# Performance work log

Hardware: AMD Instinct MI355X
Metric: run time of the kernel (lower is better)

Reference implementation:

```python
import jax, jax.numpy as jnp
import numpy as np
import math

R = 16            # input_resolution (window side)
N = R * R         # tokens per window
H = 16            # num_heads
D = 32            # head_dim
SCALE = D ** -0.5

def _rel_pos_index(r):
    # Swin-style relative position index, [N, N] int
    coords = np.stack(np.meshgrid(np.arange(r), np.arange(r), indexing='ij'))  # [2,r,r]
    cf = coords.reshape(2, -1)                          # [2, N]
    rel = cf[:, :, None] - cf[:, None, :]               # [2, N, N]
    rel = rel.transpose(1, 2, 0).astype(np.int64)       # [N, N, 2]
    rel[:, :, 0] += r - 1
    rel[:, :, 1] += r - 1
    rel[:, :, 0] *= 2 * r - 1
    return rel.sum(-1)                                  # [N, N]

def _modulation(n, k):
    # cosine-distance modulation matrix, [n*n, n*n]
    idx = np.arange(n * n)
    rr, cc = idx // n, idx % n
    d = np.sqrt((rr[:, None] - rr[None, :]) ** 2 + (cc[:, None] - cc[None, :]) ** 2)
    T = 4 * (n - 1) * math.sqrt(2)
    f = 2 * math.pi / T
    m = np.exp(np.cos(f * d)) / 2
    if k % n == 0:
        k = k - 1
    bound = m[0, k]
    m = np.where(m < bound, 0.0, m)
    return jnp.asarray(m, jnp.float32)

_REL_IDX = jnp.asarray(_rel_pos_index(R))   # [N, N] int
_MOD = _modulation(R, 3 * R)                 # [N, N] float (eval-mode local modulation)

def setup_inputs() -> dict:
    key = jax.random.key(0)
    ks = jax.random.split(key, 6)
    C = H * D
    return {
        'x': jax.random.normal(ks[0], (128, N, C), jnp.float32),
        'qkv_w': jax.random.normal(ks[1], (3 * C, C), jnp.float32) * 0.02,
        'qkv_b': jax.random.normal(ks[2], (3 * C,), jnp.float32) * 0.02,
        'proj_w': jax.random.normal(ks[3], (C, C), jnp.float32) * 0.02,
        'proj_b': jax.random.normal(ks[4], (C,), jnp.float32) * 0.02,
        'rpb_table': jax.random.normal(ks[5], ((2 * R - 1) ** 2, H), jnp.float32) * 0.02,
    }

def reference(x, qkv_w, qkv_b, proj_w, proj_b, rpb_table):
    B, n, C = x.shape
    # qkv projection: torch Linear is x @ W^T + b
    qkv = x @ qkv_w.T + qkv_b                       # [B, N, 3C]
    qkv = qkv.reshape(B, n, 3, H, D)
    q = qkv[:, :, 0].transpose(0, 2, 1, 3) * SCALE  # [B, H, N, D]
    k = qkv[:, :, 1].transpose(0, 2, 1, 3)
    v = qkv[:, :, 2].transpose(0, 2, 1, 3)
    attn = jnp.einsum('bhnd,bhmd->bhnm', q, k)      # [B, H, N, N]
    bias = rpb_table[_REL_IDX]                      # [N, N, H]
    attn = attn + bias.transpose(2, 0, 1)[None]     # + [1, H, N, N]
    attn = jax.nn.softmax(attn, axis=-1)
    attn = attn * _MOD[None, None]                  # local eval-mode modulation
    out = jnp.einsum('bhnm,bhmd->bhnd', attn, v)    # [B, H, N, D]
    out = out.transpose(0, 2, 1, 3).reshape(B, n, C)
    return out @ proj_w.T + proj_b
```

## Files before the change

kernel.cpp:

```cpp
#include <hip/hip_runtime.h>
#include <hip/hip_bf16.h>

typedef unsigned short u16;
typedef unsigned int u32;
typedef __bf16 bf16x8 __attribute__((ext_vector_type(8)));
typedef float f32x4 __attribute__((ext_vector_type(4)));

#define AS1(p) ((const __attribute__((address_space(1))) void*)(p))
#define AS3(p) ((__attribute__((address_space(3))) void*)(p))

#define TOK   256
#define CDIM  512
#define QKVC  1536
#define LOG2E 1.4426950408889634f
#define QSCALE (0.17677669529663687f * 1.4426950408889634f)

__device__ __forceinline__ u16 f2b(float f) {
  unsigned u = __float_as_uint(f);
  unsigned r = (u + 0x7fffu + ((u >> 16) & 1u)) >> 16;
  return (u16)r;
}
__device__ __forceinline__ u16 f2bc(float f) {
  __bf16 h = (__bf16)f;
  u16 u;
  __builtin_memcpy(&u, &h, 2);
  return u;
}
__device__ __forceinline__ float bf_lo(u32 wd) { return __uint_as_float(wd << 16); }
__device__ __forceinline__ float bf_hi(u32 wd) { return __uint_as_float(wd & 0xffff0000u); }
__device__ __forceinline__ float ex2(float x) {
  float r;
  asm("v_exp_f32 %0, %1" : "=v"(r) : "v"(x));
  return r;
}

__global__ __launch_bounds__(256) void cvt_bf16_kernel(const float* __restrict__ in,
                                                       u16* __restrict__ out, int n) {
  int i = (blockIdx.x * 256 + threadIdx.x) * 8;
  if (i >= n) return;
  float4 a = *(const float4*)(in + i);
  float4 b = *(const float4*)(in + i + 4);
  u16 h[8];
  h[0] = f2b(a.x); h[1] = f2b(a.y); h[2] = f2b(a.z); h[3] = f2b(a.w);
  h[4] = f2b(b.x); h[5] = f2b(b.y); h[6] = f2b(b.z); h[7] = f2b(b.w);
  *(uint4*)(out + i) = *(const uint4*)h;
}

__global__ __launch_bounds__(256) void build_bias2_kernel(const float* __restrict__ rpb,
                                                          u16* __restrict__ bias2) {
  int i = blockIdx.x * 256 + threadIdx.x;
  int tr = i & 63, lane = (i >> 6) & 63, rb = (i >> 12) & 15, h = i >> 16;
  int t = tr >> 2, r = tr & 3;
  int n = rb * 16 + (lane & 15);
  int m = t * 16 + (lane >> 4) * 4 + r;
  int idx = ((n >> 4) - (m >> 4) + 15) * 31 + ((n & 15) - (m & 15) + 15);
  bias2[i] = f2b(rpb[idx * 16 + h] * LOG2E);
}

__global__ __launch_bounds__(256) void build_mod2_kernel(u16* __restrict__ mod2) {
  int i = blockIdx.x * 256 + threadIdx.x;
  int tr = i & 63, lane = (i >> 6) & 63, rb = i >> 12;
  int t = tr >> 2, r = tr & 3;
  int n = rb * 16 + (lane & 15);
  int m = t * 16 + (lane >> 4) * 4 + r;
  int dr = (n >> 4) - (m >> 4), dc = (n & 15) - (m & 15);
  int d2 = dr * dr + dc * dc;
  float val = 0.0f;
  if (d2 <= 229) {
    const float fc = 6.2831853071795864f / (60.0f * 1.4142135623730951f);
    val = expf(cosf(fc * sqrtf((float)d2))) * 0.5f;
  }
  mod2[i] = f2b(val);
}

template<int MODE>
__global__ __launch_bounds__(MODE == 0 ? 512 : 256) void gemm_bt(
    const float* __restrict__ Ax, const u16* __restrict__ A,
    const u16* __restrict__ Bt, const float* __restrict__ bvec,
    u16* __restrict__ oq, u16* __restrict__ ok, u16* __restrict__ ov,
    float* __restrict__ of) {
  constexpr int K = 512;
  constexpr int BM = (MODE == 0) ? 256 : 128;
  constexpr int NT = (MODE == 0) ? 512 : 256;
  constexpr int NBN = (MODE == 0) ? 12 : 4;
  constexpr int PER_XCD = (MODE == 0) ? 192 : 128;
  __shared__ __align__(16) u16 SM[(MODE == 0) ? 32768 : 16384];
  u16* As = SM;
  u16* Bs = SM + BM * 64;
  const int tid = threadIdx.x, lane = tid & 63, w = tid >> 6;
  const int wr = w >> 1, wc = w & 1, lr = lane & 15, lg = lane >> 4;
  const int logical = (blockIdx.x & 7) * PER_XCD + (blockIdx.x >> 3);
  const int bm = (logical / (2 * NBN)) * 2 + (logical & 1);
  const int bn = (logical % (2 * NBN)) >> 1;
  const u16* Bg = Bt + (size_t)bn * 128 * K;
  f32x4 acc[4][4];
#pragma unroll
  for (int m = 0; m < 4; ++m)
#pragma unroll
    for (int n = 0; n < 4; ++n) acc[m][n] = (f32x4){0.f, 0.f, 0.f, 0.f};

  for (int k0 = 0; k0 < K; k0 += 64) {
    if (MODE == 0) {
#pragma unroll
      for (int it = 0; it < 4; ++it) {
        int chunk = it * NT + tid;
        int r = chunk >> 3, kc = chunk & 7;
        int gg = kc ^ (r & 7);
        const float* src = Ax + (size_t)(bm * 256 + r) * K + k0 + gg * 8;
        float4 v0 = *(const float4*)src;
        float4 v1 = *(const float4*)(src + 4);
        u16 hb[8];
        hb[0] = f2bc(v0.x); hb[1] = f2bc(v0.y); hb[2] = f2bc(v0.z); hb[3] = f2bc(v0.w);
        hb[4] = f2bc(v1.x); hb[5] = f2bc(v1.y); hb[6] = f2bc(v1.z); hb[7] = f2bc(v1.w);
        *(uint4*)(As + chunk * 8) = *(const uint4*)hb;
      }
#pragma unroll
      for (int it = 0; it < 2; ++it) {
        int chunk = it * NT + tid;
        int r = chunk >> 3, kc = chunk & 7;
        int kcs = kc ^ (r & 7);
        __builtin_amdgcn_global_load_lds(AS1(Bg + (size_t)r * K + k0 + kcs * 8),
                                         AS3(Bs + chunk * 8), 16, 0, 0);
      }
    } else {
      const u16* Ag = A + (size_t)bm * 128 * K;
#pragma unroll
      for (int it = 0; it < 4; ++it) {
        int chunk = it * NT + tid;
        int r = chunk >> 3, kc = chunk & 7;
        int kcs = kc ^ (r & 7);
        __builtin_amdgcn_global_load_lds(AS1(Ag + (size_t)r * K + k0 + kcs * 8),
                                         AS3(As + chunk * 8), 16, 0, 0);
        __builtin_amdgcn_global_load_lds(AS1(Bg + (size_t)r * K + k0 + kcs * 8),
                                         AS3(Bs + chunk * 8), 16, 0, 0);
      }
    }
    __syncthreads();
#pragma unroll
    for (int kk = 0; kk < 2; ++kk) {
      bf16x8 a[4], b[4];
#pragma unroll
      for (int m = 0; m < 4; ++m) {
        int ar = wr * 64 + m * 16 + lr;
        a[m] = *(const bf16x8*)&As[ar * 64 + (((kk * 4 + lg) ^ (lr & 7)) << 3)];
      }
#pragma unroll
      for (int n = 0; n < 4; ++n) {
        int br = wc * 64 + n * 16 + lr;
        b[n] = *(const bf16x8*)&Bs[br * 64 + (((kk * 4 + lg) ^ (lr & 7)) << 3)];
      }
#pragma unroll
      for (int m = 0; m < 4; ++m)
#pragma unroll
        for (int n = 0; n < 4; ++n)
          acc[m][n] = __builtin_amdgcn_mfma_f32_16x16x32_bf16(a[m], b[n], acc[m][n], 0, 0, 0);
    }
    __syncthreads();
  }

  if (MODE == 1) {
#pragma unroll
    for (int m = 0; m < 4; ++m)
#pragma unroll
      for (int n = 0; n < 4; ++n)
#pragma unroll
        for (int r = 0; r < 4; ++r) {
          int row = bm * BM + wr * 64 + m * 16 + lg * 4 + r;
          int col = bn * 128 + wc * 64 + n * 16 + lr;
          of[(size_t)row * CDIM + col] = acc[m][n][r] + bvec[col];
        }
    return;
  }

  const int typ = bn >> 2;
  const int col0 = bn * 128 + wc * 64;
  const int row0 = bm * 256 + wr * 64;
  char* Tb = (char*)SM + w * 8192;

#pragma unroll
  for (int n = 0; n < 4; ++n) {
    float bv = bvec[col0 + n * 16 + lr];
#pragma unroll
    for (int m = 0; m < 4; ++m)
#pragma unroll
      for (int r = 0; r < 4; ++r) {
        float v = acc[m][n][r] + bv;
        if (typ == 0) v *= QSCALE;
        int row_l, col_l;
        if (typ < 2) { row_l = m * 16 + lg * 4 + r; col_l = n * 16 + lr; }
        else         { row_l = n * 16 + lr;         col_l = m * 16 + lg * 4 + r; }
        int byte = row_l * 128 + ((((col_l >> 3) ^ (row_l & 7)) << 4) | ((col_l & 7) << 1));
        *(u16*)(Tb + byte) = f2b(v);
      }
  }
  asm volatile("" ::: "memory");
  if (typ < 2) {
    int tok = row0 + lane;
    int tokb = tok >> 8;
    u16* obase = (typ == 0) ? oq : ok;
#pragma unroll
    for (int G = 0; G < 8; ++G) {
      int hl = G >> 2, q = G & 3;
      uint4 v = *(const uint4*)(Tb + lane * 128 + ((G ^ (lane & 7)) << 4));
      int hh = ((col0 >> 5) & 15) + hl;
      size_t a = ((((size_t)tokb * 16 + hh) * 16 + ((tok >> 4) & 15)) * 64 +
                  ((tok & 15) | (q << 4))) * 8;
      *(uint4*)(obase + a) = v;
    }
  } else {
    int tl0 = row0 & 255, tokb = row0 >> 8;
    int hl = lane >> 5, t = (lane >> 3) & 3, c = lane & 7;
    int hh = ((col0 >> 5) & 15) + hl;
#pragma unroll
    for (int i = 0; i < 8; ++i) {
      int d = i * 4 + t;
      uint4 v = *(const uint4*)(Tb + (hl * 32 + d) * 128 + (c << 4));
      size_t a = (((size_t)tokb * 16 + hh) * 32 + d) * 256 + tl0 + c * 8;
      *(uint4*)(ov + a) = v;
    }
  }
}

__global__ __launch_bounds__(512, 4) void attn_kernel(const u16* __restrict__ qfrag,
                                                      const u16* __restrict__ kfrag,
                                                      const u16* __restrict__ vsw,
                                                      const u16* __restrict__ bias2,
                                                      const u16* __restrict__ mod2,
                                                      u16* __restrict__ attnout) {
  __shared__ __align__(16) u16 SM[24576];
  const int logical = (blockIdx.x & 7) * 512 + (blockIdx.x >> 3);
  const int h = logical >> 8;
  const int b = (logical >> 1) & 127;
  const int qpair = logical & 1;
  const int tid = threadIdx.x, lane = tid & 63, w = tid >> 6;
  const int lr = lane & 15, lg = lane >> 4;
  const int rb = qpair * 8 + w;
  const int bhid = b * 16 + h;

  const u16* kg = kfrag + (size_t)bhid * 8192;
  const u16* vg = vsw + (size_t)bhid * 8192;
#pragma unroll
  for (int it = 0; it < 2; ++it) {
    __builtin_amdgcn_global_load_lds(AS1(kg + (it * 512 + tid) * 8),
                                     AS3(SM + (it * 512 + tid) * 8), 16, 0, 0);
    __builtin_amdgcn_global_load_lds(AS1(vg + (it * 512 + tid) * 8),
                                     AS3(SM + 8192 + (it * 512 + tid) * 8), 16, 0, 0);
  }
  bf16x8 qf = *(const bf16x8*)(qfrag + ((size_t)bhid * 16 + rb) * 512 + lane * 8);
  __syncthreads();

  const u16* bias_base = bias2 + (((size_t)h * 16 + rb) * 64 + lane) * 64;
  const u16* mod_base  = mod2 + ((size_t)rb * 64 + lane) * 64;
  char* Pbase = (char*)SM + 32768 + w * 2048;
  const char* Vb = (const char*)(SM + 8192);

  f32x4 s[16];
#pragma unroll
  for (int q = 0; q < 4; ++q) {
    u32 bw8[8];
    {
      const uint4* bp = (const uint4*)(bias_base + q * 16);
      *(uint4*)&bw8[0] = bp[0]; *(uint4*)&bw8[4] = bp[1];
    }
#pragma unroll
    for (int tl = 0; tl < 4; ++tl) {
      int t = q * 4 + tl;
      bf16x8 kf = *(const bf16x8*)(SM + (t * 64 + lane) * 8);
      f32x4 c;
      c[0] = bf_lo(bw8[tl * 2]);     c[1] = bf_hi(bw8[tl * 2]);
      c[2] = bf_lo(bw8[tl * 2 + 1]); c[3] = bf_hi(bw8[tl * 2 + 1]);
      s[t] = __builtin_amdgcn_mfma_f32_16x16x32_bf16(kf, qf, c, 0, 0, 0);
    }
  }

  float mr0 = s[0][0], mr1 = s[0][1], mr2 = s[0][2], mr3 = s[0][3];
#pragma unroll
  for (int t = 1; t < 16; ++t) {
    mr0 = fmaxf(mr0, s[t][0]); mr1 = fmaxf(mr1, s[t][1]);
    mr2 = fmaxf(mr2, s[t][2]); mr3 = fmaxf(mr3, s[t][3]);
  }
  float mx = fmaxf(fmaxf(mr0, mr1), fmaxf(mr2, mr3));
  mx = fmaxf(mx, __shfl_xor(mx, 16, 64));
  mx = fmaxf(mx, __shfl_xor(mx, 32, 64));
  float s0 = 0.f, s1 = 0.f, s2 = 0.f, s3 = 0.f;
#pragma unroll
  for (int t = 0; t < 16; ++t) {
    s[t][0] = ex2(s[t][0] - mx); s0 += s[t][0];
    s[t][1] = ex2(s[t][1] - mx); s1 += s[t][1];
    s[t][2] = ex2(s[t][2] - mx); s2 += s[t][2];
    s[t][3] = ex2(s[t][3] - mx); s3 += s[t][3];
  }
  float sm = (s0 + s1) + (s2 + s3);
  sm += __shfl_xor(sm, 16, 64);
  sm += __shfl_xor(sm, 32, 64);
  sm = __builtin_amdgcn_rcpf(sm);

  f32x4 o0 = (f32x4){0.f, 0.f, 0.f, 0.f};
  f32x4 o1 = (f32x4){0.f, 0.f, 0.f, 0.f};
#pragma unroll
  for (int q = 0; q < 4; ++q) {
    u32 mw8[8];
    {
      const uint4* mp = (const uint4*)(mod_base + q * 16);
      *(uint4*)&mw8[0] = mp[0]; *(uint4*)&mw8[4] = mp[1];
    }
#pragma unroll
    for (int tl = 0; tl < 4; ++tl) {
      int t = q * 4 + tl;
      u16 pk[4];
#pragma unroll
      for (int r = 0; r < 4; ++r) {
        u32 wd = mw8[tl * 2 + (r >> 1)];
        float mf = (r & 1) ? bf_hi(wd) : bf_lo(wd);
        pk[r] = f2bc(s[t][r] * sm * mf);
      }
      int hi2 = (t * 2 + (lg >> 1)) & 3;
      *(uint2*)(Pbase + ((t >> 1) & 1) * 1024 + ((hi2 << 4) | lr) * 16 + (lg & 1) * 8)
          = *(const uint2*)pk;
    }
    asm volatile("" ::: "memory");
#pragma unroll
    for (int kl = 0; kl < 2; ++kl) {
      bf16x8 pa = *(const bf16x8*)(Pbase + kl * 1024 + lane * 16);
      int cv = ((q * 2 + kl) * 4 + lg) ^ (lr & 7);
      bf16x8 v0 = *(const bf16x8*)(Vb + lr * 512 + cv * 16);
      bf16x8 v1 = *(const bf16x8*)(Vb + (16 + lr) * 512 + cv * 16);
      o0 = __builtin_amdgcn_mfma_f32_16x16x32_bf16(pa, v0, o0, 0, 0, 0);
      o1 = __builtin_amdgcn_mfma_f32_16x16x32_bf16(pa, v1, o1, 0, 0, 0);
    }
    asm volatile("" ::: "memory");
  }

  u16* orow = attnout + (size_t)(b * TOK + rb * 16) * CDIM + h * 32;
#pragma unroll
  for (int r = 0; r < 4; ++r) {
    orow[(size_t)(lg * 4 + r) * CDIM + lr] = f2bc(o0[r]);
    orow[(size_t)(lg * 4 + r) * CDIM + 16 + lr] = f2bc(o1[r]);
  }
}

extern "C" void kernel_launch(void* const* d_in, const int* in_sizes, int n_in,
                              void* d_out, int out_size, void* d_ws, size_t ws_size,
                              hipStream_t stream) {
  const float* x      = (const float*)d_in[0];
  const float* qkv_w  = (const float*)d_in[1];
  const float* qkv_b  = (const float*)d_in[2];
  const float* proj_w = (const float*)d_in[3];
  const float* proj_b = (const float*)d_in[4];
  const float* rpb    = (const float*)d_in[5];

  char* ws = (char*)d_ws;
  u16* qkvwb  = (u16*)(ws + 33554432);
  u16* projwb = (u16*)(ws + 35127296);
  u16* qfrag  = (u16*)(ws + 35651584);
  u16* kfrag  = (u16*)(ws + 69206016);
  u16* vswb   = (u16*)(ws + 102760448);
  u16* attnb  = (u16*)(ws + 136314880);
  u16* bias2  = (u16*)(ws + 169869312);
  u16* mod2   = (u16*)(ws + 171966464);

  cvt_bf16_kernel<<<384, 256, 0, stream>>>(qkv_w, qkvwb, 1536 * 512);
  cvt_bf16_kernel<<<128, 256, 0, stream>>>(proj_w, projwb, 512 * 512);
  build_bias2_kernel<<<4096, 256, 0, stream>>>(rpb, bias2);
  build_mod2_kernel<<<256, 256, 0, stream>>>(mod2);

  gemm_bt<0><<<1536, 512, 0, stream>>>(x, nullptr, qkvwb, qkv_b,
                                       qfrag, kfrag, vswb, nullptr);
  attn_kernel<<<4096, 512, 0, stream>>>(qfrag, kfrag, vswb, bias2, mod2, attnb);
  gemm_bt<1><<<1024, 256, 0, stream>>>(nullptr, attnb, projwb, proj_b,
                                       nullptr, nullptr, nullptr, (float*)d_out);
}
```

Baseline: 214.6 us.

## Software-pipeline QKV GEMM with register prefetch of x and double-buffered weight tiles

In the QKV projection GEMM (MODE 0), the next k-step's fp32 activation tile is prefetched into registers and the next weight tile is loaded asynchronously into a second LDS buffer while MFMAs run on the current step. This is meant to hide global load latency behind compute instead of stalling at each k-step. It raises register pressure from holding 8 float4 per thread and uses LDS space that was previously unused. The output-projection GEMM path is unchanged apart from renaming.

```diff
diff --git a/kernel.cpp b/kernel.cpp
--- a/kernel.cpp
+++ b/kernel.cpp
@@ -86,7 +86,8 @@
   constexpr int PER_XCD = (MODE == 0) ? 192 : 128;
   __shared__ __align__(16) u16 SM[(MODE == 0) ? 32768 : 16384];
   u16* As = SM;
-  u16* Bs = SM + BM * 64;
+  u16* Bs0 = SM + BM * 64;
+  u16* Bs1 = (MODE == 0) ? (SM + BM * 64 + 8192) : Bs0;
   const int tid = threadIdx.x, lane = tid & 63, w = tid >> 6;
   const int wr = w >> 1, wc = w & 1, lr = lane & 15, lg = lane >> 4;
   const int logical = (blockIdx.x & 7) * PER_XCD + (blockIdx.x >> 3);
@@ -99,63 +100,111 @@
 #pragma unroll
     for (int n = 0; n < 4; ++n) acc[m][n] = (f32x4){0.f, 0.f, 0.f, 0.f};
 
-  for (int k0 = 0; k0 < K; k0 += 64) {
-    if (MODE == 0) {
+  if (MODE == 0) {
+    float4 ar0[4], ar1[4];
+#pragma unroll
+    for (int it = 0; it < 4; ++it) {
+      int chunk = it * NT + tid;
+      int r = chunk >> 3, gg = (chunk & 7) ^ (r & 7);
+      const float* src = Ax + (size_t)(bm * 256 + r) * K + gg * 8;
+      ar0[it] = *(const float4*)src;
+      ar1[it] = *(const float4*)(src + 4);
+    }
+#pragma unroll
+    for (int it = 0; it < 2; ++it) {
+      int chunk = it * NT + tid;
+      int r = chunk >> 3, kcs = (chunk & 7) ^ (r & 7);
+      __builtin_amdgcn_global_load_lds(AS1(Bg + (size_t)r * K + kcs * 8),
+                                       AS3(Bs0 + chunk * 8), 16, 0, 0);
+    }
+#pragma unroll 1
+    for (int ks = 0; ks < 8; ++ks) {
+      const int k0 = ks * 64;
+      u16* Bcur = (ks & 1) ? Bs1 : Bs0;
+      u16* Bnxt = (ks & 1) ? Bs0 : Bs1;
 #pragma unroll
       for (int it = 0; it < 4; ++it) {
         int chunk = it * NT + tid;
-        int r = chunk >> 3, kc = chunk & 7;
-        int gg = kc ^ (r & 7);
-        const float* src = Ax + (size_t)(bm * 256 + r) * K + k0 + gg * 8;
-        float4 v0 = *(const float4*)src;
-        float4 v1 = *(const float4*)(src + 4);
         u16 hb[8];
-        hb[0] = f2bc(v0.x); hb[1] = f2bc(v0.y); hb[2] = f2bc(v0.z); hb[3] = f2bc(v0.w);
-        hb[4] = f2bc(v1.x); hb[5] = f2bc(v1.y); hb[6] = f2bc(v1.z); hb[7] = f2bc(v1.w);
+        hb[0] = f2bc(ar0[it].x); hb[1] = f2bc(ar0[it].y);
+        hb[2] = f2bc(ar0[it].z); hb[3] = f2bc(ar0[it].w);
+        hb[4] = f2bc(ar1[it].x); hb[5] = f2bc(ar1[it].y);
+        hb[6] = f2bc(ar1[it].z); hb[7] = f2bc(ar1[it].w);
         *(uint4*)(As + chunk * 8) = *(const uint4*)hb;
       }
-#pragma unroll
-      for (int it = 0; it < 2; ++it) {
-        int chunk = it * NT + tid;
-        int r = chunk >> 3, kc = chunk & 7;
-        int kcs = kc ^ (r & 7);
-        __builtin_amdgcn_global_load_lds(AS1(Bg + (size_t)r * K + k0 + kcs * 8),
-                                         AS3(Bs + chunk * 8), 16, 0, 0);
-      }
-    } else {
-      const u16* Ag = A + (size_t)bm * 128 * K;
+      __syncthreads();
+      if (ks < 7) {
+#pragma unroll
+        for (int it = 0; it < 2; ++it) {
+          int chunk = it * NT + tid;
+          int r = chunk >> 3, kcs = (chunk & 7) ^ (r & 7);
+          __builtin_amdgcn_global_load_lds(AS1(Bg + (size_t)r * K + k0 + 64 + kcs * 8),
+                                           AS3(Bnxt + chunk * 8), 16, 0, 0);
+        }
+#pragma unroll
+        for (int it = 0; it < 4; ++it) {
+          int chunk = it * NT + tid;
+          int r = chunk >> 3, gg = (chunk & 7) ^ (r & 7);
+          const float* src = Ax + (size_t)(bm * 256 + r) * K + k0 + 64 + gg * 8;
+          ar0[it] = *(const float4*)src;
+          ar1[it] = *(const float4*)(src + 4);
+        }
+      }
+#pragma unroll
+      for (int kk = 0; kk < 2; ++kk) {
+        bf16x8 a[4], b[4];
+#pragma unroll
+        for (int m = 0; m < 4; ++m) {
+          int ar = wr * 64 + m * 16 + lr;
+          a[m] = *(const bf16x8*)&As[ar * 64 + (((kk * 4 + lg) ^ (lr & 7)) << 3)];
+        }
+#pragma unroll
+        for (int n = 0; n < 4; ++n) {
+          int br = wc * 64 + n * 16 + lr;
+          b[n] = *(const bf16x8*)&Bcur[br * 64 + (((kk * 4 + lg) ^ (lr & 7)) << 3)];
+        }
+#pragma unroll
+        for (int m = 0; m < 4; ++m)
+#pragma unroll
+          for (int n = 0; n < 4; ++n)
+            acc[m][n] = __builtin_amdgcn_mfma_f32_16x16x32_bf16(a[m], b[n], acc[m][n], 0, 0, 0);
+      }
+      __syncthreads();
+    }
+  } else {
+    const u16* Ag = A + (size_t)bm * 128 * K;
+    for (int k0 = 0; k0 < K; k0 += 64) {
 #pragma unroll
       for (int it = 0; it < 4; ++it) {
         int chunk = it * NT + tid;
-        int r = chunk >> 3, kc = chunk & 7;
-        int kcs = kc ^ (r & 7);
+        int r = chunk >> 3, kcs = (chunk & 7) ^ (r & 7);
         __builtin_amdgcn_global_load_lds(AS1(Ag + (size_t)r * K + k0 + kcs * 8),
                                          AS3(As + chunk * 8), 16, 0, 0);
         __builtin_amdgcn_global_load_lds(AS1(Bg + (size_t)r * K + k0 + kcs * 8),
-                                         AS3(Bs + chunk * 8), 16, 0, 0);
-      }
-    }
-    __syncthreads();
-#pragma unroll
-    for (int kk = 0; kk < 2; ++kk) {
-      bf16x8 a[4], b[4];
-#pragma unroll
-      for (int m = 0; m < 4; ++m) {
-        int ar = wr * 64 + m * 16 + lr;
-        a[m] = *(const bf16x8*)&As[ar * 64 + (((kk * 4 + lg) ^ (lr & 7)) << 3)];
-      }
-#pragma unroll
-      for (int n = 0; n < 4; ++n) {
-        int br = wc * 64 + n * 16 + lr;
-        b[n] = *(const bf16x8*)&Bs[br * 64 + (((kk * 4 + lg) ^ (lr & 7)) << 3)];
-      }
-#pragma unroll
-      for (int m = 0; m < 4; ++m)
-#pragma unroll
-        for (int n = 0; n < 4; ++n)
-          acc[m][n] = __builtin_amdgcn_mfma_f32_16x16x32_bf16(a[m], b[n], acc[m][n], 0, 0, 0);
-    }
-    __syncthreads();
+                                         AS3(Bs0 + chunk * 8), 16, 0, 0);
+      }
+      __syncthreads();
+#pragma unroll
+      for (int kk = 0; kk < 2; ++kk) {
+        bf16x8 a[4], b[4];
+#pragma unroll
+        for (int m = 0; m < 4; ++m) {
+          int ar = wr * 64 + m * 16 + lr;
+          a[m] = *(const bf16x8*)&As[ar * 64 + (((kk * 4 + lg) ^ (lr & 7)) << 3)];
+        }
+#pragma unroll
+        for (int n = 0; n < 4; ++n) {
+          int br = wc * 64 + n * 16 + lr;
+          b[n] = *(const bf16x8*)&Bs0[br * 64 + (((kk * 4 + lg) ^ (lr & 7)) << 3)];
+        }
+#pragma unroll
+        for (int m = 0; m < 4; ++m)
+#pragma unroll
+          for (int n = 0; n < 4; ++n)
+            acc[m][n] = __builtin_amdgcn_mfma_f32_16x16x32_bf16(a[m], b[n], acc[m][n], 0, 0, 0);
+      }
+      __syncthreads();
+    }
   }
 
   if (MODE == 1) {
```

Result: slower. 227.2 us (+5.9%).

## Stream fp32 activations into LDS asynchronously and convert to bf16 at fragment load

Applied to the files above, without the earlier changes.

The QKV GEMM previously loaded fp32 x through registers, converted it to bf16 and stored it to LDS, using 256-row tiles with 512 threads. Now fp32 tiles are copied straight into swizzled LDS with global_load_lds, and each fragment is converted to bf16 just before the MFMA. The tile drops to 128x128 with 256 threads and two blocks per CU, and the grid doubles. This removes the register round-trip and synchronous global loads, at the cost of twice the LDS traffic for A and repeated conversion work for every wave that reads the same rows.

```diff
diff --git a/kernel.cpp b/kernel.cpp
--- a/kernel.cpp
+++ b/kernel.cpp
@@ -74,19 +74,18 @@
 }
 
 template<int MODE>
-__global__ __launch_bounds__(MODE == 0 ? 512 : 256) void gemm_bt(
+__global__ __launch_bounds__(256, 2) void gemm_bt(
     const float* __restrict__ Ax, const u16* __restrict__ A,
     const u16* __restrict__ Bt, const float* __restrict__ bvec,
     u16* __restrict__ oq, u16* __restrict__ ok, u16* __restrict__ ov,
     float* __restrict__ of) {
   constexpr int K = 512;
-  constexpr int BM = (MODE == 0) ? 256 : 128;
-  constexpr int NT = (MODE == 0) ? 512 : 256;
   constexpr int NBN = (MODE == 0) ? 12 : 4;
-  constexpr int PER_XCD = (MODE == 0) ? 192 : 128;
-  __shared__ __align__(16) u16 SM[(MODE == 0) ? 32768 : 16384];
-  u16* As = SM;
-  u16* Bs = SM + BM * 64;
+  constexpr int PER_XCD = (MODE == 0) ? 384 : 128;
+  __shared__ __align__(16) char SMc[(MODE == 0) ? 49152 : 32768];
+  float* Af = (float*)SMc;
+  u16* As = (u16*)SMc;
+  u16* Bs = (MODE == 0) ? (u16*)(SMc + 32768) : (u16*)(SMc + 16384);
   const int tid = threadIdx.x, lane = tid & 63, w = tid >> 6;
   const int wr = w >> 1, wc = w & 1, lr = lane & 15, lg = lane >> 4;
   const int logical = (blockIdx.x & 7) * PER_XCD + (blockIdx.x >> 3);
@@ -99,63 +98,86 @@
 #pragma unroll
     for (int n = 0; n < 4; ++n) acc[m][n] = (f32x4){0.f, 0.f, 0.f, 0.f};
 
-  for (int k0 = 0; k0 < K; k0 += 64) {
-    if (MODE == 0) {
+  if (MODE == 0) {
+    const float* Abase = Ax + (size_t)(bm * 128) * K;
+    for (int k0 = 0; k0 < K; k0 += 64) {
+#pragma unroll
+      for (int it = 0; it < 8; ++it) {
+        int chunk = it * 256 + tid;
+        int r = chunk >> 4, g = chunk & 15;
+        int gg = g ^ (r & 7);
+        __builtin_amdgcn_global_load_lds(AS1(Abase + (size_t)r * K + k0 + gg * 4),
+                                         AS3((char*)Af + chunk * 16), 16, 0, 0);
+      }
 #pragma unroll
       for (int it = 0; it < 4; ++it) {
-        int chunk = it * NT + tid;
-        int r = chunk >> 3, kc = chunk & 7;
-        int gg = kc ^ (r & 7);
-        const float* src = Ax + (size_t)(bm * 256 + r) * K + k0 + gg * 8;
-        float4 v0 = *(const float4*)src;
-        float4 v1 = *(const float4*)(src + 4);
-        u16 hb[8];
-        hb[0] = f2bc(v0.x); hb[1] = f2bc(v0.y); hb[2] = f2bc(v0.z); hb[3] = f2bc(v0.w);
-        hb[4] = f2bc(v1.x); hb[5] = f2bc(v1.y); hb[6] = f2bc(v1.z); hb[7] = f2bc(v1.w);
-        *(uint4*)(As + chunk * 8) = *(const uint4*)hb;
-      }
-#pragma unroll
-      for (int it = 0; it < 2; ++it) {
-        int chunk = it * NT + tid;
-        int r = chunk >> 3, kc = chunk & 7;
-        int kcs = kc ^ (r & 7);
+        int chunk = it * 256 + tid;
+        int r = chunk >> 3, kcs = (chunk & 7) ^ (r & 7);
         __builtin_amdgcn_global_load_lds(AS1(Bg + (size_t)r * K + k0 + kcs * 8),
                                          AS3(Bs + chunk * 8), 16, 0, 0);
       }
-    } else {
-      const u16* Ag = A + (size_t)bm * 128 * K;
+      __syncthreads();
+#pragma unroll
+      for (int kk = 0; kk < 2; ++kk) {
+        bf16x8 a[4], b[4];
+#pragma unroll
+        for (int m = 0; m < 4; ++m) {
+          int ar = wr * 64 + m * 16 + lr;
+          int G = kk * 8 + lg * 2;
+          const char* rbase = (const char*)Af + ar * 256;
+          float4 f0 = *(const float4*)(rbase + ((G ^ (ar & 7)) << 4));
+          float4 f1 = *(const float4*)(rbase + (((G + 1) ^ (ar & 7)) << 4));
+          u16 ha[8] = {f2bc(f0.x), f2bc(f0.y), f2bc(f0.z), f2bc(f0.w),
+                       f2bc(f1.x), f2bc(f1.y), f2bc(f1.z), f2bc(f1.w)};
+          __builtin_memcpy(&a[m], ha, 16);
+        }
+#pragma unroll
+        for (int n = 0; n < 4; ++n) {
+          int br = wc * 64 + n * 16 + lr;
+          b[n] = *(const bf16x8*)&Bs[br * 64 + (((kk * 4 + lg) ^ (lr & 7)) << 3)];
+        }
+#pragma unroll
+        for (int m = 0; m < 4; ++m)
+#pragma unroll
+          for (int n = 0; n < 4; ++n)
+            acc[m][n] = __builtin_amdgcn_mfma_f32_16x16x32_bf16(a[m], b[n], acc[m][n], 0, 0, 0);
+      }
+      __syncthreads();
+    }
+  } else {
+    const u16* Ag = A + (size_t)bm * 128 * K;
+    for (int k0 = 0; k0 < K; k0 += 64) {
 #pragma unroll
       for (int it = 0; it < 4; ++it) {
-        int chunk = it * NT + tid;
-        int r = chunk >> 3, kc = chunk & 7;
-        int kcs = kc ^ (r & 7);
+        int chunk = it * 256 + tid;
+        int r = chunk >> 3, kcs = (chunk & 7) ^ (r & 7);
         __builtin_amdgcn_global_load_lds(AS1(Ag + (size_t)r * K + k0 + kcs * 8),
                                          AS3(As + chunk * 8), 16, 0, 0);
         __builtin_amdgcn_global_load_lds(AS1(Bg + (size_t)r * K + k0 + kcs * 8),
                                          AS3(Bs + chunk * 8), 16, 0, 0);
       }
-    }
-    __syncthreads();
-#pragma unroll
-    for (int kk = 0; kk < 2; ++kk) {
-      bf16x8 a[4], b[4];
-#pragma unroll
-      for (int m = 0; m < 4; ++m) {
-        int ar = wr * 64 + m * 16 + lr;
-        a[m] = *(const bf16x8*)&As[ar * 64 + (((kk * 4 + lg) ^ (lr & 7)) << 3)];
-      }
-#pragma unroll
-      for (int n = 0; n < 4; ++n) {
-        int br = wc * 64 + n * 16 + lr;
-        b[n] = *(const bf16x8*)&Bs[br * 64 + (((kk * 4 + lg) ^ (lr & 7)) << 3)];
-      }
-#pragma unroll
-      for (int m = 0; m < 4; ++m)
-#pragma unroll
-        for (int n = 0; n < 4; ++n)
-          acc[m][n] = __builtin_amdgcn_mfma_f32_16x16x32_bf16(a[m], b[n], acc[m][n], 0, 0, 0);
-    }
-    __syncthreads();
+      __syncthreads();
+#pragma unroll
+      for (int kk = 0; kk < 2; ++kk) {
+        bf16x8 a[4], b[4];
+#pragma unroll
+        for (int m = 0; m < 4; ++m) {
+          int ar = wr * 64 + m * 16 + lr;
+          a[m] = *(const bf16x8*)&As[ar * 64 + (((kk * 4 + lg) ^ (lr & 7)) << 3)];
+        }
+#pragma unroll
+        for (int n = 0; n < 4; ++n) {
+          int br = wc * 64 + n * 16 + lr;
+          b[n] = *(const bf16x8*)&Bs[br * 64 + (((kk * 4 + lg) ^ (lr & 7)) << 3)];
+        }
+#pragma unroll
+        for (int m = 0; m < 4; ++m)
+#pragma unroll
+          for (int n = 0; n < 4; ++n)
+            acc[m][n] = __builtin_amdgcn_mfma_f32_16x16x32_bf16(a[m], b[n], acc[m][n], 0, 0, 0);
+      }
+      __syncthreads();
+    }
   }
 
   if (MODE == 1) {
@@ -165,7 +187,7 @@
       for (int n = 0; n < 4; ++n)
 #pragma unroll
         for (int r = 0; r < 4; ++r) {
-          int row = bm * BM + wr * 64 + m * 16 + lg * 4 + r;
+          int row = bm * 128 + wr * 64 + m * 16 + lg * 4 + r;
           int col = bn * 128 + wc * 64 + n * 16 + lr;
           of[(size_t)row * CDIM + col] = acc[m][n][r] + bvec[col];
         }
@@ -174,8 +196,8 @@
 
   const int typ = bn >> 2;
   const int col0 = bn * 128 + wc * 64;
-  const int row0 = bm * 256 + wr * 64;
-  char* Tb = (char*)SM + w * 8192;
+  const int row0 = bm * 128 + wr * 64;
+  char* Tb = SMc + w * 8192;
 
 #pragma unroll
   for (int n = 0; n < 4; ++n) {
@@ -364,7 +386,7 @@
   build_bias2_kernel<<<4096, 256, 0, stream>>>(rpb, bias2);
   build_mod2_kernel<<<256, 256, 0, stream>>>(mod2);
 
-  gemm_bt<0><<<1536, 512, 0, stream>>>(x, nullptr, qkvwb, qkv_b,
+  gemm_bt<0><<<3072, 256, 0, stream>>>(x, nullptr, qkvwb, qkv_b,
                                        qfrag, kfrag, vswb, nullptr);
   attn_kernel<<<4096, 512, 0, stream>>>(qfrag, kfrag, vswb, bias2, mod2, attnb);
   gemm_bt<1><<<1024, 256, 0, stream>>>(nullptr, attnb, projwb, proj_b,
```

Result: slower. 226.6 us (+5.6%).
